# Kernel optimization log

Measured on AMD Instinct MI355X. Metric: run time of the kernel, lower is better.

The kernel has to match this reference:

```python
import jax, jax.numpy as jnp
import numpy as np

NUM_BINS = 64
R = 2                      # kernel_radius = ceil(2*sigma), sigma=1
NB = NUM_BINS + 2 * R      # 68 padded bins
EPS = 1e-8


def _bspline(d):
    # cubic B-spline Parzen kernel, sigma=1 so d/sigma == d
    ad = jnp.abs(d)
    return jnp.where(
        ad < 1.0, (3.0 * ad ** 3 - 6.0 * ad ** 2 + 4.0) / 6.0,
        jnp.where(ad < 2.0, (2.0 - ad) ** 3 / 6.0, jnp.zeros_like(ad)))


def setup_inputs() -> dict:
    key = jax.random.key(0)
    k1, k2 = jax.random.split(key)
    shape = (2, 1, 80, 80, 80)
    source = jax.random.normal(k1, shape, dtype=jnp.float32)
    target = jax.random.normal(k2, shape, dtype=jnp.float32)
    return {"source": source, "target": target}


def _win(x):
    # x: [B, N] flattened voxels (mask=None, sample_rate=1 keeps all voxels)
    # returns win_idx [B, 2R, N] int32 and bspline weights [B, 2R, N]
    mx = jax.lax.stop_gradient(jnp.max(x, axis=1))            # [B]
    mn = jax.lax.stop_gradient(jnp.min(x, axis=1))            # [B]
    bw = (mx - mn) / NUM_BINS                                 # bin width
    pad_min = mn - bw * R
    pos = (x - pad_min[:, None]) / bw[:, None]                # [B, N]
    idx = jax.lax.stop_gradient(
        jnp.clip(jnp.floor(pos), R, R + NUM_BINS - 1))        # detached floor+clamp
    min_win = (idx - R + 1).astype(jnp.int32)                 # [B, N]
    r = jnp.arange(2 * R, dtype=jnp.int32)                    # [2R]
    win_idx = min_win[:, None, :] + r[None, :, None]          # [B, 2R, N]
    # bin_center is arange(NB), so gathered centers == win_idx as float
    w = _bspline(pos[:, None, :] - win_idx.astype(x.dtype))   # [B, 2R, N]
    return win_idx, w


def _densify(win_idx, w):
    # scatter-add window weights into dense [B, NB, N] bin-weight matrix.
    # (Equivalent to the torch eq-mask-and-sum loop: window indices are distinct.)
    B, _, N = w.shape
    col = jnp.broadcast_to(jnp.arange(N), win_idx.shape[1:])  # [2R, N]
    def per_b(ib, wb):
        return jnp.zeros((NB, N), wb.dtype).at[ib, col].add(wb)
    return jax.vmap(per_b)(win_idx, w)


def reference(source, target):
    B = source.shape[0]
    s = source.reshape(B, -1)   # [B, N]
    t = target.reshape(B, -1)
    si, sw = _win(s)
    ti, tw = _win(t)
    sbw = _densify(si, sw)      # [B, NB, N]
    tbw = _densify(ti, tw)      # [B, NB, N]
    source_hist = sbw.sum(-1)   # [B, NB]
    target_hist = tbw.sum(-1)
    joint_hist = jnp.einsum('bin,bjn->bij', sbw, tbw)   # [B, NB, NB]
    source_density = source_hist / jnp.maximum(source_hist.sum(-1, keepdims=True), EPS)
    target_density = target_hist / jnp.maximum(target_hist.sum(-1, keepdims=True), EPS)
    joint_density = joint_hist / jnp.maximum(joint_hist.sum(axis=(1, 2), keepdims=True), EPS)
    return (source_density, target_density, joint_density)
```

## Files before the change

kernel.cpp:

```cpp
#include <hip/hip_runtime.h>
#include <float.h>

#define NB 68
#define NJ (NB * NB)
#define NSLICE 4
#define HTPB 1024
#define MMBLK 125
#define SCALE 16384.0f
#define LHSZ (2 * NJ + 8)


__global__ __launch_bounds__(1024) void k_prep(const float* __restrict__ src,
                                               const float* __restrict__ tgt,
                                               float4* __restrict__ P,
                                               unsigned* __restrict__ J,
                                               int n4) {
    __shared__ float red[16][4];
    const int b = blockIdx.y;
    const int lin = (b * gridDim.x + blockIdx.x) * 1024 + threadIdx.x;
    if (lin < NSLICE * 2 * NJ) J[lin] = 0u;

    const int i = blockIdx.x * 1024 + threadIdx.x;
    float smx = -FLT_MAX, smn = FLT_MAX, tmx = -FLT_MAX, tmn = FLT_MAX;
    if (i < n4) {
        float4 v = ((const float4*)src)[(size_t)b * n4 + i];
        float4 w = ((const float4*)tgt)[(size_t)b * n4 + i];
        smx = fmaxf(fmaxf(v.x, v.y), fmaxf(v.z, v.w));
        smn = fminf(fminf(v.x, v.y), fminf(v.z, v.w));
        tmx = fmaxf(fmaxf(w.x, w.y), fmaxf(w.z, w.w));
        tmn = fminf(fminf(w.x, w.y), fminf(w.z, w.w));
    }
#pragma unroll
    for (int m = 1; m < 64; m <<= 1) {
        smx = fmaxf(smx, __shfl_xor(smx, m));
        smn = fminf(smn, __shfl_xor(smn, m));
        tmx = fmaxf(tmx, __shfl_xor(tmx, m));
        tmn = fminf(tmn, __shfl_xor(tmn, m));
    }
    const int wave = threadIdx.x >> 6;
    if ((threadIdx.x & 63) == 0) {
        red[wave][0] = smx;
        red[wave][1] = smn;
        red[wave][2] = tmx;
        red[wave][3] = tmn;
    }
    __syncthreads();
    if (threadIdx.x == 0) {
#pragma unroll
        for (int k = 1; k < 16; ++k) {
            smx = fmaxf(smx, red[k][0]);
            smn = fminf(smn, red[k][1]);
            tmx = fmaxf(tmx, red[k][2]);
            tmn = fminf(tmn, red[k][3]);
        }
        P[b * 128 + blockIdx.x] = make_float4(smx, smn, tmx, tmn);
    }
}

__device__ __forceinline__ float bspl(float d) {
    float ad = fabsf(d);
    float a = (3.0f * ad * ad * ad - 6.0f * ad * ad + 4.0f) * (1.0f / 6.0f);
    float t = 2.0f - ad;
    float c = t * t * t * (1.0f / 6.0f);
    return ad < 1.0f ? a : (ad < 2.0f ? c : 0.0f);
}

__device__ __forceinline__ void vox1(float sv, float tv, unsigned* lh,
                                     float spad, float sinv, float tpad,
                                     float tinv) {
    float posS = (sv - spad) * sinv;
    float fS = floorf(posS);
    fS = fminf(fmaxf(fS, 2.0f), 65.0f);
    int si = (int)fS - 1;
    float dS = posS - fS;
    float a[4] = {bspl(dS + 1.0f), bspl(dS), bspl(dS - 1.0f), bspl(dS - 2.0f)};

    float posT = (tv - tpad) * tinv;
    float fT = floorf(posT);
    fT = fminf(fmaxf(fT, 2.0f), 65.0f);
    int ti = (int)fT - 1;
    float dT = posT - fT;
    float b0 = bspl(dT + 1.0f), b1 = bspl(dT), b2 = bspl(dT - 1.0f),
          b3 = bspl(dT - 2.0f);

    unsigned* base = lh + ((ti & 1) ? (NJ + 1) : 0) + si * NB + ti;
#pragma unroll
    for (int r = 0; r < 4; ++r) {
        unsigned q0 = (unsigned)(a[r] * b0 * SCALE + 0.5f);
        unsigned q1 = (unsigned)(a[r] * b1 * SCALE + 0.5f);
        unsigned q2 = (unsigned)(a[r] * b2 * SCALE + 0.5f);
        unsigned q3 = (unsigned)(a[r] * b3 * SCALE + 0.5f);
        atomicAdd((unsigned long long*)(base + r * NB),
                  (unsigned long long)q0 | ((unsigned long long)q1 << 32));
        atomicAdd((unsigned long long*)(base + r * NB + 2),
                  (unsigned long long)q2 | ((unsigned long long)q3 << 32));
    }
}

__global__ __launch_bounds__(HTPB) void k_hist(
    const float* __restrict__ src, const float* __restrict__ tgt,
    const float4* __restrict__ P, unsigned* __restrict__ J, int n4) {
    __shared__ __align__(16) unsigned lh[LHSZ];
    __shared__ float pmm[8], mmv[4];
    const int tid = threadIdx.x;
    const int b = blockIdx.y;

    if (tid < 128) {
        float smx = -FLT_MAX, smn = FLT_MAX, tmx = -FLT_MAX, tmn = FLT_MAX;
        if (tid < MMBLK) {
            float4 v = P[b * 128 + tid];
            smx = v.x; smn = v.y; tmx = v.z; tmn = v.w;
        }
#pragma unroll
        for (int m = 1; m < 64; m <<= 1) {
            smx = fmaxf(smx, __shfl_xor(smx, m));
            smn = fminf(smn, __shfl_xor(smn, m));
            tmx = fmaxf(tmx, __shfl_xor(tmx, m));
            tmn = fminf(tmn, __shfl_xor(tmn, m));
        }
        if ((tid & 63) == 0) {
            int w = tid >> 6;
            pmm[w * 4 + 0] = smx;
            pmm[w * 4 + 1] = smn;
            pmm[w * 4 + 2] = tmx;
            pmm[w * 4 + 3] = tmn;
        }
    }
    uint4* z4 = (uint4*)lh;
    const uint4 zz = make_uint4(0u, 0u, 0u, 0u);
    for (int i = tid; i < LHSZ / 4; i += HTPB) z4[i] = zz;
    __syncthreads();
    if (tid == 0) {
        mmv[0] = fmaxf(pmm[0], pmm[4]);
        mmv[1] = fminf(pmm[1], pmm[5]);
        mmv[2] = fmaxf(pmm[2], pmm[6]);
        mmv[3] = fminf(pmm[3], pmm[7]);
    }
    __syncthreads();

    const float sbw = (mmv[0] - mmv[1]) * (1.0f / 64.0f);
    const float tbw = (mmv[2] - mmv[3]) * (1.0f / 64.0f);
    const float sinv = 1.0f / sbw, tinv = 1.0f / tbw;
    const float spad = mmv[1] - 2.0f * sbw;
    const float tpad = mmv[3] - 2.0f * tbw;

    const int i0 = blockIdx.x * HTPB + tid;
    if (i0 < n4) {
        float4 sA = ((const float4*)src)[(size_t)b * n4 + i0];
        float4 tA = ((const float4*)tgt)[(size_t)b * n4 + i0];
        vox1(sA.x, tA.x, lh, spad, sinv, tpad, tinv);
        vox1(sA.y, tA.y, lh, spad, sinv, tpad, tinv);
        vox1(sA.z, tA.z, lh, spad, sinv, tpad, tinv);
        vox1(sA.w, tA.w, lh, spad, sinv, tpad, tinv);
    }
    __syncthreads();

    const int rot = (blockIdx.x * 1327) % NJ;
    unsigned* Jb = J + ((size_t)(blockIdx.x & (NSLICE - 1)) * 2 + b) * NJ;
    for (int k = tid; k < NJ; k += HTPB) {
        int i = k + rot;
        if (i >= NJ) i -= NJ;
        unsigned s = lh[i] + lh[NJ + 1 + i];
        if (s) atomicAdd(&Jb[i], s);
    }
}

__global__ __launch_bounds__(1024) void k_norm(
    const unsigned* __restrict__ J, float* __restrict__ out, double inv) {
    __shared__ float jf[NJ];
    __shared__ float part[NB][8];
    const int b = blockIdx.x;
    const int tid = threadIdx.x;

    for (int i = tid; i < NJ; i += 1024) {
        unsigned s = 0u;
#pragma unroll
        for (int sl = 0; sl < NSLICE; ++sl)
            s += J[((size_t)sl * 2 + b) * NJ + i];
        float f = (float)((double)s * inv);
        jf[i] = f;
        out[4 * NB + b * NJ + i] = f;
    }
    __syncthreads();

    if (tid < 8 * NB) {
        int r = tid >> 3, k = tid & 7;
        float s = 0.0f;
#pragma unroll
        for (int j = 0; j < 9; ++j) {
            int c = k + 8 * j;
            if (c < NB) s += jf[r * NB + c];
        }
        part[r][k] = s;
    }
    __syncthreads();
    if (tid < NB) {
        float s = part[tid][0] + part[tid][1] + part[tid][2] + part[tid][3] +
                  part[tid][4] + part[tid][5] + part[tid][6] + part[tid][7];
        out[b * NB + tid] = s;
    }
    __syncthreads();

    if (tid < 8 * NB) {
        int c = tid >> 3, k = tid & 7;
        float s = 0.0f;
#pragma unroll
        for (int j = 0; j < 9; ++j) {
            int r = k + 8 * j;
            if (r < NB) s += jf[r * NB + c];
        }
        part[c][k] = s;
    }
    __syncthreads();
    if (tid < NB) {
        float s = part[tid][0] + part[tid][1] + part[tid][2] + part[tid][3] +
                  part[tid][4] + part[tid][5] + part[tid][6] + part[tid][7];
        out[2 * NB + b * NB + tid] = s;
    }
}

extern "C" void kernel_launch(void* const* d_in, const int* in_sizes, int n_in,
                              void* d_out, int out_size, void* d_ws,
                              size_t ws_size, hipStream_t stream) {
    const float* src = (const float*)d_in[0];
    const float* tgt = (const float*)d_in[1];
    float* out = (float*)d_out;
    float4* P = (float4*)((char*)d_ws + 64);
    unsigned* J = (unsigned*)((char*)d_ws + 4160);
    const int nvox = in_sizes[0] / 2;
    const int n4 = nvox / 4;
    const double inv = 1.0 / ((double)nvox * (double)SCALE);

    k_prep<<<dim3(MMBLK, 2), dim3(1024), 0, stream>>>(src, tgt, P, J, n4);
    k_hist<<<dim3(MMBLK, 2), dim3(HTPB), 0, stream>>>(src, tgt, P, J, n4);
    k_norm<<<dim3(2), dim3(1024), 0, stream>>>(J, out, inv);
}
```

Baseline: 22.22 us.

## Fuse normalization into histogram kernel via last-block atomic counter

```diff
diff --git a/kernel.cpp b/kernel.cpp
--- a/kernel.cpp
+++ b/kernel.cpp
@@ -14,11 +14,13 @@
                                                const float* __restrict__ tgt,
                                                float4* __restrict__ P,
                                                unsigned* __restrict__ J,
+                                               unsigned* __restrict__ ctr,
                                                int n4) {
     __shared__ float red[16][4];
     const int b = blockIdx.y;
     const int lin = (b * gridDim.x + blockIdx.x) * 1024 + threadIdx.x;
     if (lin < NSLICE * 2 * NJ) J[lin] = 0u;
+    else if (lin == NSLICE * 2 * NJ) { ctr[0] = 0u; ctr[1] = 0u; }
 
     const int i = blockIdx.x * 1024 + threadIdx.x;
     float smx = -FLT_MAX, smn = FLT_MAX, tmx = -FLT_MAX, tmn = FLT_MAX;
@@ -99,9 +101,11 @@
 
 __global__ __launch_bounds__(HTPB) void k_hist(
     const float* __restrict__ src, const float* __restrict__ tgt,
-    const float4* __restrict__ P, unsigned* __restrict__ J, int n4) {
+    const float4* __restrict__ P, unsigned* __restrict__ J,
+    unsigned* __restrict__ ctr, float* __restrict__ out, double inv, int n4) {
     __shared__ __align__(16) unsigned lh[LHSZ];
     __shared__ float pmm[8], mmv[4];
+    __shared__ unsigned lastFlag;
     const int tid = threadIdx.x;
     const int b = blockIdx.y;
 
@@ -163,20 +167,21 @@
         unsigned s = lh[i] + lh[NJ + 1 + i];
         if (s) atomicAdd(&Jb[i], s);
     }
-}
-
-__global__ __launch_bounds__(1024) void k_norm(
-    const unsigned* __restrict__ J, float* __restrict__ out, double inv) {
-    __shared__ float jf[NJ];
-    __shared__ float part[NB][8];
-    const int b = blockIdx.x;
-    const int tid = threadIdx.x;
-
-    for (int i = tid; i < NJ; i += 1024) {
+    __syncthreads();
+
+    if (tid == 0)
+        lastFlag = (atomicAdd(&ctr[b], 1u) == (unsigned)(MMBLK - 1)) ? 1u : 0u;
+    __syncthreads();
+    if (!lastFlag) return;
+
+    float* jf = (float*)lh;
+    float* part = (float*)(lh + NJ + 16);
+    for (int i = tid; i < NJ; i += HTPB) {
         unsigned s = 0u;
 #pragma unroll
         for (int sl = 0; sl < NSLICE; ++sl)
-            s += J[((size_t)sl * 2 + b) * NJ + i];
+            s += __hip_atomic_load(&J[((size_t)sl * 2 + b) * NJ + i],
+                                   __ATOMIC_RELAXED, __HIP_MEMORY_SCOPE_AGENT);
         float f = (float)((double)s * inv);
         jf[i] = f;
         out[4 * NB + b * NJ + i] = f;
@@ -191,12 +196,13 @@
             int c = k + 8 * j;
             if (c < NB) s += jf[r * NB + c];
         }
-        part[r][k] = s;
+        part[r * 8 + k] = s;
     }
     __syncthreads();
     if (tid < NB) {
-        float s = part[tid][0] + part[tid][1] + part[tid][2] + part[tid][3] +
-                  part[tid][4] + part[tid][5] + part[tid][6] + part[tid][7];
+        float s = part[tid * 8 + 0] + part[tid * 8 + 1] + part[tid * 8 + 2] +
+                  part[tid * 8 + 3] + part[tid * 8 + 4] + part[tid * 8 + 5] +
+                  part[tid * 8 + 6] + part[tid * 8 + 7];
         out[b * NB + tid] = s;
     }
     __syncthreads();
@@ -209,12 +215,13 @@
             int r = k + 8 * j;
             if (r < NB) s += jf[r * NB + c];
         }
-        part[c][k] = s;
+        part[c * 8 + k] = s;
     }
     __syncthreads();
     if (tid < NB) {
-        float s = part[tid][0] + part[tid][1] + part[tid][2] + part[tid][3] +
-                  part[tid][4] + part[tid][5] + part[tid][6] + part[tid][7];
+        float s = part[tid * 8 + 0] + part[tid * 8 + 1] + part[tid * 8 + 2] +
+                  part[tid * 8 + 3] + part[tid * 8 + 4] + part[tid * 8 + 5] +
+                  part[tid * 8 + 6] + part[tid * 8 + 7];
         out[2 * NB + b * NB + tid] = s;
     }
 }
@@ -225,13 +232,14 @@
     const float* src = (const float*)d_in[0];
     const float* tgt = (const float*)d_in[1];
     float* out = (float*)d_out;
+    unsigned* ctr = (unsigned*)d_ws;
     float4* P = (float4*)((char*)d_ws + 64);
     unsigned* J = (unsigned*)((char*)d_ws + 4160);
     const int nvox = in_sizes[0] / 2;
     const int n4 = nvox / 4;
     const double inv = 1.0 / ((double)nvox * (double)SCALE);
 
-    k_prep<<<dim3(MMBLK, 2), dim3(1024), 0, stream>>>(src, tgt, P, J, n4);
-    k_hist<<<dim3(MMBLK, 2), dim3(HTPB), 0, stream>>>(src, tgt, P, J, n4);
-    k_norm<<<dim3(2), dim3(1024), 0, stream>>>(J, out, inv);
-}
+    k_prep<<<dim3(MMBLK, 2), dim3(1024), 0, stream>>>(src, tgt, P, J, ctr, n4);
+    k_hist<<<dim3(MMBLK, 2), dim3(HTPB), 0, stream>>>(src, tgt, P, J, ctr, out,
+                                                      inv, n4);
+}
```

New measurement: 22.85 us. 2.8% more time.
